# Kernel tuning notes

Measured on AMD Instinct MI355X. Metric: run time of the kernel, lower is better.

The kernel has to match this reference:

```python
import jax, jax.numpy as jnp
import numpy as np

EMBED_DIM = 1024
NUM_HEADS = 16
HEAD_DIM = EMBED_DIM // NUM_HEADS


def _rope_tables(seq_len, dim, dtype):
    # inv_freq over even indices of head_dim
    inv_freq = 1.0 / (10000.0 ** (jnp.arange(0, dim, 2, dtype=jnp.float32) / dim))
    t = jnp.arange(seq_len, dtype=jnp.float32)
    freqs = jnp.einsum('i,j->ij', t, inv_freq)            # [S, dim/2]
    emb = jnp.concatenate([freqs, freqs], axis=-1)        # [S, dim]
    return jnp.cos(emb).astype(dtype)[None], jnp.sin(emb).astype(dtype)[None]  # [1,S,dim]


def _rotate_half(x):
    x1, x2 = jnp.split(x, 2, axis=-1)
    return jnp.concatenate([-x2, x1], axis=-1)


def _apply_rope(x, cos, sin):
    return x * cos + _rotate_half(x) * sin


def setup_inputs() -> dict:
    key = jax.random.key(0)
    ks = jax.random.split(key, 9)
    S, B, E = 2048, 2, EMBED_DIM
    sc = 1.0 / np.sqrt(E)
    inp = {
        'query': jax.random.normal(ks[0], (S, B, E), jnp.float32),
        'Wq': jax.random.normal(ks[1], (E, E), jnp.float32) * sc,
        'bq': jnp.zeros((E,), jnp.float32),
        'Wk': jax.random.normal(ks[2], (E, E), jnp.float32) * sc,
        'bk': jnp.zeros((E,), jnp.float32),
        'Wv': jax.random.normal(ks[3], (E, E), jnp.float32) * sc,
        'bv': jnp.zeros((E,), jnp.float32),
        'Wo': jax.random.normal(ks[4], (E, E), jnp.float32) * sc,
        'bo': jnp.zeros((E,), jnp.float32),
    }
    return inp


def reference(query, Wq, bq, Wk, bk, Wv, bv, Wo, bo):
    tgt_len, bsz, E = query.shape
    H, hd = NUM_HEADS, HEAD_DIM
    scaling = hd ** (-0.5)

    # self-attention projections (torch Linear: x @ W.T + b)
    q = (query @ Wq.T + bq) * scaling
    k = query @ Wk.T + bk
    v = query @ Wv.T + bv

    # [S, B, E] -> [B*H, S, hd]
    def to_heads(x):
        return x.reshape(tgt_len, bsz * H, hd).transpose(1, 0, 2)

    q, k, v = to_heads(q), to_heads(k), to_heads(v)

    cos, sin = _rope_tables(tgt_len, hd, q.dtype)  # [1,S,hd]
    q = _apply_rope(q, cos, sin)
    k = _apply_rope(k, cos, sin)

    attn_weights = jnp.einsum('bqd,bkd->bqk', q, k)       # [B*H, S, S]
    attn_probs = jax.nn.softmax(attn_weights, axis=-1)
    attn = jnp.einsum('bqk,bkd->bqd', attn_probs, v)      # [B*H, S, hd]

    attn = attn.transpose(1, 0, 2).reshape(tgt_len, bsz, E)
    return attn @ Wo.T + bo
```

## Files before the change

### kernel.cpp

```cpp
#include <hip/hip_runtime.h>
#include <hip/hip_bf16.h>


typedef short shortx8 __attribute__((ext_vector_type(8)));
typedef float floatx4 __attribute__((ext_vector_type(4)));
typedef float floatx16 __attribute__((ext_vector_type(16)));

#define S_LEN 2048
#define BATCH 2
#define EMB 1024
#define NH 16
#define HD 64
#define BH 32
#define MROWS 4096
#define HEAD_STRIDE (S_LEN*HD)

#define QSCALE 0.1803368801111204f

#if __has_builtin(__builtin_amdgcn_exp2f)
#define EXP2(x) __builtin_amdgcn_exp2f(x)
#else
#define EXP2(x) exp2f(x)
#endif

__device__ __forceinline__ float b2f(unsigned short u) {
    union { unsigned int i; float f; } v; v.i = ((unsigned int)u) << 16; return v.f;
}
__device__ __forceinline__ unsigned short f2b(float f) {
    union { float f; unsigned int i; } v; v.f = f;
    unsigned int x = v.i;
    return (unsigned short)((x + 0x7fffu + ((x >> 16) & 1u)) >> 16);
}
__device__ __forceinline__ unsigned short f2b_fast(float f) {
    union { float f; unsigned int i; } v; v.f = f;
    return (unsigned short)((v.i + 0x8000u) >> 16);
}
__device__ __forceinline__ unsigned int fbits(float f) {
    union { float f; unsigned int i; } v; v.f = f; return v.i;
}
__device__ __forceinline__ unsigned int pack_bf16_2(float lo, float hi) {
    return __builtin_amdgcn_perm(fbits(hi) + 0x8000u, fbits(lo) + 0x8000u, 0x07060302u);
}
__device__ __forceinline__ shortx8 cvt8(const float* p) {
    floatx4 a = *(const floatx4*)p;
    floatx4 b = *(const floatx4*)(p + 4);
    shortx8 r;
    r[0] = (short)f2b(a[0]); r[1] = (short)f2b(a[1]);
    r[2] = (short)f2b(a[2]); r[3] = (short)f2b(a[3]);
    r[4] = (short)f2b(b[0]); r[5] = (short)f2b(b[1]);
    r[6] = (short)f2b(b[2]); r[7] = (short)f2b(b[3]);
    return r;
}
__device__ __forceinline__ shortx8 cvt8f(const float* p) {
    floatx4 a = *(const floatx4*)p;
    floatx4 b = *(const floatx4*)(p + 4);
    union { uint4 u; shortx8 s; } r;
    r.u.x = pack_bf16_2(a[0], a[1]);
    r.u.y = pack_bf16_2(a[2], a[3]);
    r.u.z = pack_bf16_2(b[0], b[1]);
    r.u.w = pack_bf16_2(b[2], b[3]);
    return r.s;
}
__device__ __forceinline__ void g2l16(const unsigned short* g, unsigned short* l) {
    __builtin_amdgcn_global_load_lds(
        (const __attribute__((address_space(1))) unsigned int*)(const void*)g,
        (__attribute__((address_space(3))) unsigned int*)(void*)l, 16, 0, 0);
}

__global__ __launch_bounds__(256) void prep(
    const float* __restrict__ X,
    const float* __restrict__ Wq, const float* __restrict__ Wk,
    const float* __restrict__ Wv,
    unsigned short* __restrict__ Xb, unsigned short* __restrict__ Wb,
    float* __restrict__ rtab)
{
    const int g = blockIdx.x * 256 + threadIdx.x;
    if (g < 65536) {
        const int s = g >> 5, j = g & 31;
        const float inv = expf(-(float)j * (9.210340371976184f / 32.0f));
        const float ang = (float)s * inv;
        rtab[s * 64 + j]      = cosf(ang);
        rtab[s * 64 + 32 + j] = sinf(ang);
    } else if (g < 458752) {
        const int h = g - 65536;
        const int seg = h >> 17;
        const int idx = (h & 131071) * 8;
        const float* W = (seg == 0) ? Wq : (seg == 1) ? Wk : Wv;
        *(shortx8*)&Wb[seg * 1048576 + idx] = cvt8(&W[idx]);
    } else {
        const int idx = (g - 458752) * 8;
        *(shortx8*)&Xb[idx] = cvt8(&X[idx]);
    }
}

__device__ __forceinline__ void qkv_epilogue(
    floatx4 (&acc)[4][4], int mat, int m0, int nn0, int wm, int wn,
    int qm, int quad, const float* bias, const float* rtab,
    unsigned short* dst)
{
    if (mat == 2) {
#pragma unroll
        for (int i = 0; i < 4; i++) {
#pragma unroll
            for (int j = 0; j < 4; j++) {
                const int colg = nn0 + wn + j * 16 + qm;
                const float bv_ = bias[colg];
                const int h = colg >> 6, d = colg & 63;
#pragma unroll
                for (int r = 0; r < 4; r++) {
                    const int rowg = m0 + wm + i * 16 + quad * 4 + r;
                    const int s = rowg >> 1, b = rowg & 1;
                    dst[((b * NH + h) * HD + d) * S_LEN + s] = f2b(acc[i][j][r] + bv_);
                }
            }
        }
    } else {
        const float scale = (mat == 0) ? QSCALE : 1.0f;
#pragma unroll
        for (int i = 0; i < 4; i++) {
#pragma unroll
            for (int jp = 0; jp < 2; jp++) {
                const int c1 = nn0 + wn + jp * 16 + qm;
                const float b1 = bias[c1], b2 = bias[c1 + 32];
                const int h = c1 >> 6;
                const int d1 = c1 & 63;
#pragma unroll
                for (int r = 0; r < 4; r++) {
                    const int rowg = m0 + wm + i * 16 + quad * 4 + r;
                    const int s = rowg >> 1, b = rowg & 1;
                    const float cs = rtab[s * 64 + d1];
                    const float sn = rtab[s * 64 + d1 + 32];
                    const float x1 = (acc[i][jp][r] + b1) * scale;
                    const float x2 = (acc[i][jp + 2][r] + b2) * scale;
                    unsigned short* base = &dst[((b * NH + h) * S_LEN + s) * HD];
                    base[d1]      = f2b(x1 * cs - x2 * sn);
                    base[d1 + 32] = f2b(x2 * cs + x1 * sn);
                }
            }
        }
    }
}

__global__ __launch_bounds__(256) void qkv_gemm_gl(
    const unsigned short* __restrict__ Xb,
    const unsigned short* __restrict__ Wb,
    const float* __restrict__ bq, const float* __restrict__ bk,
    const float* __restrict__ bv,
    const float* __restrict__ rtab,
    unsigned short* __restrict__ Qh, unsigned short* __restrict__ Kh,
    unsigned short* __restrict__ Vt)
{
    __shared__ unsigned short At[128 * 64];
    __shared__ unsigned short Bt[128 * 64];

    const int tid  = threadIdx.x;
    const int wave = tid >> 6, lane = tid & 63;
    const int wm = (wave >> 1) * 64, wn = (wave & 1) * 64;
    const int qm = lane & 15, quad = lane >> 4;

    const int m0  = blockIdx.x * 128;
    const int n0g = blockIdx.y * 128;
    const int mat = n0g >> 10;
    const int nn0 = n0g & 1023;

    const unsigned short* W = Wb + (size_t)mat * 1048576;
    const float* bias = (mat == 0) ? bq : (mat == 1) ? bk : bv;
    unsigned short* dst = (mat == 0) ? Qh : (mat == 1) ? Kh : Vt;

    floatx4 acc[4][4] = {};

    const int xs = qm & 7;

    for (int k0 = 0; k0 < EMB; k0 += 64) {
#pragma unroll
        for (int c = 0; c < 4; c++) {
            const int e   = (c * 256 + tid) * 8;
            const int row = e >> 6;
            const int gcol = (((e >> 3) & 7) ^ (row & 7)) * 8;
            g2l16(&Xb[(m0 + row) * EMB + k0 + gcol], &At[e]);
            g2l16(&W[(nn0 + row) * EMB + k0 + gcol], &Bt[e]);
        }
        __syncthreads();

#pragma unroll
        for (int kk = 0; kk < 2; kk++) {
            shortx8 a[4], b[4];
#pragma unroll
            for (int i = 0; i < 4; i++)
                a[i] = *(shortx8*)&At[(wm + i * 16 + qm) * 64 + (((kk * 4 + quad) ^ xs) * 8)];
#pragma unroll
            for (int j = 0; j < 4; j++)
                b[j] = *(shortx8*)&Bt[(wn + j * 16 + qm) * 64 + (((kk * 4 + quad) ^ xs) * 8)];
#pragma unroll
            for (int i = 0; i < 4; i++)
#pragma unroll
                for (int j = 0; j < 4; j++)
                    acc[i][j] = __builtin_amdgcn_mfma_f32_16x16x32_bf16(a[i], b[j], acc[i][j], 0, 0, 0);
        }
        __syncthreads();
    }

    qkv_epilogue(acc, mat, m0, nn0, wm, wn, qm, quad, bias, rtab, dst);
}

#define LDB 72

__global__ __launch_bounds__(256) void qkv_gemm_fb(
    const float* __restrict__ X,
    const unsigned short* __restrict__ Wb,
    const float* __restrict__ bq, const float* __restrict__ bk,
    const float* __restrict__ bv,
    const float* __restrict__ rtab,
    unsigned short* __restrict__ Qh, unsigned short* __restrict__ Kh,
    unsigned short* __restrict__ Vt)
{
    __shared__ unsigned short At[128 * LDB];
    __shared__ unsigned short Bt[128 * LDB];

    const int tid  = threadIdx.x;
    const int wave = tid >> 6, lane = tid & 63;
    const int wm = (wave >> 1) * 64, wn = (wave & 1) * 64;
    const int qm = lane & 15, quad = lane >> 4;

    const int m0  = blockIdx.x * 128;
    const int n0g = blockIdx.y * 128;
    const int mat = n0g >> 10;
    const int nn0 = n0g & 1023;

    const unsigned short* W = Wb + (size_t)mat * 1048576;
    const float* bias = (mat == 0) ? bq : (mat == 1) ? bk : bv;
    unsigned short* dst = (mat == 0) ? Qh : (mat == 1) ? Kh : Vt;

    const int r0 = tid >> 3;
    const int ko = (tid & 7) * 8;

    floatx4 acc[4][4] = {};

    for (int k0 = 0; k0 < EMB; k0 += 64) {
#pragma unroll
        for (int c = 0; c < 4; c++) {
            const int row = r0 + 32 * c;
            *(shortx8*)&At[row * LDB + ko] = cvt8(&X[(m0 + row) * EMB + k0 + ko]);
            *(shortx8*)&Bt[row * LDB + ko] = *(const shortx8*)&W[(nn0 + row) * EMB + k0 + ko];
        }
        __syncthreads();

#pragma unroll
        for (int kk = 0; kk < 2; kk++) {
            shortx8 a[4], b[4];
#pragma unroll
            for (int i = 0; i < 4; i++)
                a[i] = *(shortx8*)&At[(wm + i * 16 + qm) * LDB + kk * 32 + quad * 8];
#pragma unroll
            for (int j = 0; j < 4; j++)
                b[j] = *(shortx8*)&Bt[(wn + j * 16 + qm) * LDB + kk * 32 + quad * 8];
#pragma unroll
            for (int i = 0; i < 4; i++)
#pragma unroll
                for (int j = 0; j < 4; j++)
                    acc[i][j] = __builtin_amdgcn_mfma_f32_16x16x32_bf16(a[i], b[j], acc[i][j], 0, 0, 0);
        }
        __syncthreads();
    }

    qkv_epilogue(acc, mat, m0, nn0, wm, wn, qm, quad, bias, rtab, dst);
}

#define LDK 72
#define LDV 136
#define LDP 72

__global__ __launch_bounds__(512, 4) void attn_kernel(
    unsigned short* Qh,
    const unsigned short* __restrict__ Kh,
    const unsigned short* __restrict__ Vt)
{
    __shared__ unsigned short ldsK[128 * LDK];
    __shared__ unsigned short ldsVT[64 * LDV];
    __shared__ unsigned short ldsP[8 * 32 * LDP];

    const int tid  = threadIdx.x;
    const int wave = tid >> 6, lane = tid & 63;
    const int l32 = lane & 31, half = lane >> 5;
    const int qg = wave >> 1, ks = wave & 1;
    const int bh = blockIdx.y;
    const int qrow = blockIdx.x * 128 + qg * 32;

    unsigned short* Qp = Qh + bh * HEAD_STRIDE;
    const unsigned short* Kp = Kh + bh * HEAD_STRIDE;
    const unsigned short* Vp = Vt + bh * HEAD_STRIDE;

    shortx8 aq[4];
#pragma unroll
    for (int kk = 0; kk < 4; kk++)
        aq[kk] = *(const shortx8*)&Qp[(qrow + l32) * HD + kk * 16 + half * 8];

    floatx16 od0 = {}, od1 = {};
    float l_run = 0.0f;

    unsigned short* myP = &ldsP[wave * 32 * LDP];
    const int kb = ks * 64;

    const int kr = tid >> 3, ko = (tid & 7) * 8;
    const int vr = tid >> 4, vo = (tid & 15) * 8;

    for (int kt = 0; kt < S_LEN / 128; kt++) {
        const int kbase = kt * 128;
        *(shortx8*)&ldsK[kr * LDK + ko]        = *(const shortx8*)&Kp[(kbase + kr) * HD + ko];
        *(shortx8*)&ldsK[(kr + 64) * LDK + ko] = *(const shortx8*)&Kp[(kbase + kr + 64) * HD + ko];
        *(shortx8*)&ldsVT[vr * LDV + vo]        = *(const shortx8*)&Vp[vr * S_LEN + kbase + vo];
        *(shortx8*)&ldsVT[(vr + 32) * LDV + vo] = *(const shortx8*)&Vp[(vr + 32) * S_LEN + kbase + vo];
        __syncthreads();

#pragma unroll
        for (int sub = 0; sub < 2; sub++) {
            floatx16 sc = {};
#pragma unroll
            for (int kk = 0; kk < 4; kk++) {
                const shortx8 kf =
                    *(shortx8*)&ldsK[(kb + sub * 32 + l32) * LDK + kk * 16 + half * 8];
                sc = __builtin_amdgcn_mfma_f32_32x32x16_bf16(kf, aq[kk], sc, 0, 0, 0);
            }
#pragma unroll
            for (int c = 0; c < 4; c++) {
                const float p0 = EXP2(sc[4 * c + 0]);
                const float p1 = EXP2(sc[4 * c + 1]);
                const float p2 = EXP2(sc[4 * c + 2]);
                const float p3 = EXP2(sc[4 * c + 3]);
                l_run += (p0 + p1) + (p2 + p3);
                uint2 w;
                w.x = pack_bf16_2(p0, p1);
                w.y = pack_bf16_2(p2, p3);
                *(uint2*)&myP[l32 * LDP + sub * 32 + c * 8 + 4 * half] = w;
            }
        }

#pragma unroll
        for (int kc = 0; kc < 4; kc++) {
            const shortx8 ap = *(shortx8*)&myP[l32 * LDP + kc * 16 + half * 8];
            const shortx8 v0 = *(shortx8*)&ldsVT[l32 * LDV + kb + kc * 16 + half * 8];
            const shortx8 v1 = *(shortx8*)&ldsVT[(32 + l32) * LDV + kb + kc * 16 + half * 8];
            od0 = __builtin_amdgcn_mfma_f32_32x32x16_bf16(ap, v0, od0, 0, 0, 0);
            od1 = __builtin_amdgcn_mfma_f32_32x32x16_bf16(ap, v1, od1, 0, 0, 0);
        }
        __syncthreads();
    }

    l_run += __shfl_xor(l_run, 32, 64);

    float* ltab  = (float*)ldsVT + qg * 64 + ks * 32;
    float* odbuf = (float*)ldsP + qg * 2048;
    if (half == 0) ltab[l32] = l_run;
    if (ks == 1) {
#pragma unroll
        for (int g = 0; g < 16; g++) {
            const int row = (g & 3) + 8 * (g >> 2) + 4 * half;
            odbuf[row * 64 + l32]      = od0[g];
            odbuf[row * 64 + 32 + l32] = od1[g];
        }
    }
    __syncthreads();
    if (ks == 0) {
        const float* l0 = (float*)ldsVT + qg * 64;
        const float* l1 = l0 + 32;
#pragma unroll
        for (int g = 0; g < 16; g++) {
            const int row = (g & 3) + 8 * (g >> 2) + 4 * half;
            const float inv = 1.0f / (l0[row] + l1[row]);
            const float v0 = od0[g] + odbuf[row * 64 + l32];
            const float v1 = od1[g] + odbuf[row * 64 + 32 + l32];
            Qp[(qrow + row) * HD + l32]      = f2b(v0 * inv);
            Qp[(qrow + row) * HD + 32 + l32] = f2b(v1 * inv);
        }
    }
}

__global__ __launch_bounds__(256) void out_gemm(
    const unsigned short* __restrict__ O,
    const float* __restrict__ Wo, const float* __restrict__ bo,
    float* __restrict__ out)
{
    __shared__ unsigned short At[128 * LDB];
    __shared__ unsigned short Bt[64 * LDB];

    const int tid  = threadIdx.x;
    const int wave = tid >> 6, lane = tid & 63;
    const int wm = (wave >> 1) * 64, wn = (wave & 1) * 32;
    const int qm = lane & 15, quad = lane >> 4;
    const int m0 = blockIdx.x * 128;
    const int n0 = blockIdx.y * 64;

    const int r0 = tid >> 3;
    const int ko = (tid & 7) * 8;

    floatx4 acc[4][2] = {};

    for (int k0 = 0; k0 < EMB; k0 += 64) {
        const int k = k0 + ko;
#pragma unroll
        for (int c = 0; c < 4; c++) {
            const int row = r0 + 32 * c;
            const int m = m0 + row;
            *(shortx8*)&At[row * LDB + ko] =
                *(const shortx8*)&O[(((m & 1) * NH + (k >> 6)) * S_LEN + (m >> 1)) * HD + (k & 63)];
        }
#pragma unroll
        for (int c = 0; c < 2; c++) {
            const int row = r0 + 32 * c;
            *(shortx8*)&Bt[row * LDB + ko] = cvt8f(&Wo[(n0 + row) * EMB + k]);
        }
        __syncthreads();

#pragma unroll
        for (int kk = 0; kk < 2; kk++) {
            shortx8 a[4], b[2];
#pragma unroll
            for (int i = 0; i < 4; i++)
                a[i] = *(shortx8*)&At[(wm + i * 16 + qm) * LDB + kk * 32 + quad * 8];
#pragma unroll
            for (int j = 0; j < 2; j++)
                b[j] = *(shortx8*)&Bt[(wn + j * 16 + qm) * LDB + kk * 32 + quad * 8];
#pragma unroll
            for (int i = 0; i < 4; i++)
#pragma unroll
                for (int j = 0; j < 2; j++)
                    acc[i][j] = __builtin_amdgcn_mfma_f32_16x16x32_bf16(a[i], b[j], acc[i][j], 0, 0, 0);
        }
        __syncthreads();
    }

#pragma unroll
    for (int i = 0; i < 4; i++) {
#pragma unroll
        for (int j = 0; j < 2; j++) {
            const int colg = n0 + wn + j * 16 + qm;
            const float bv_ = bo[colg];
#pragma unroll
            for (int r = 0; r < 4; r++) {
                const int rowg = m0 + wm + i * 16 + quad * 4 + r;
                out[rowg * EMB + colg] = acc[i][j][r] + bv_;
            }
        }
    }
}

extern "C" void kernel_launch(void* const* d_in, const int* in_sizes, int n_in,
                              void* d_out, int out_size, void* d_ws, size_t ws_size,
                              hipStream_t stream) {
    const float* X  = (const float*)d_in[0];
    const float* Wq = (const float*)d_in[1];
    const float* bq = (const float*)d_in[2];
    const float* Wk = (const float*)d_in[3];
    const float* bk = (const float*)d_in[4];
    const float* Wv = (const float*)d_in[5];
    const float* bv = (const float*)d_in[6];
    const float* Wo = (const float*)d_in[7];
    const float* bo = (const float*)d_in[8];
    float* out = (float*)d_out;

    unsigned short* ws = (unsigned short*)d_ws;
    unsigned short* Vt  = ws;
    unsigned short* Qh  = ws + (size_t)BH * HEAD_STRIDE;
    unsigned short* Xb  = ws + (size_t)2 * BH * HEAD_STRIDE;
    unsigned short* Kh  = (unsigned short*)d_out;
    unsigned short* Wb  = (unsigned short*)d_out + 4194304;
    float*          Rt  = (float*)d_out + 3670016;

    const bool use_xb = ws_size >= (size_t)24 * 1024 * 1024;

    prep<<<dim3(use_xb ? 3840 : 1792), 256, 0, stream>>>(X, Wq, Wk, Wv, Xb, Wb, Rt);

    if (use_xb)
        qkv_gemm_gl<<<dim3(MROWS / 128, 3 * EMB / 128), 256, 0, stream>>>(
            Xb, Wb, bq, bk, bv, Rt, Qh, Kh, Vt);
    else
        qkv_gemm_fb<<<dim3(MROWS / 128, 3 * EMB / 128), 256, 0, stream>>>(
            X, Wb, bq, bk, bv, Rt, Qh, Kh, Vt);

    attn_kernel<<<dim3(S_LEN / 128, BH), 512, 0, stream>>>(Qh, Kh, Vt);
    out_gemm<<<dim3(MROWS / 128, EMB / 64), 256, 0, stream>>>(Qh, Wo, bo, out);
}
```

Before: 203.3 us.

## Keep softmax probabilities in registers via permlane swap and XOR-swizzle LDS tiles

Drops the per-wave LDS staging buffer for the probability matrix. The exp'd scores are now packed with v_cvt_pk_bf16_f32 and rearranged across half-waves with v_permlane32_swap, so they feed the PV MFMA directly from registers. K and V^T tiles move from padded row strides to an XOR-swizzled layout, which shrinks LDS usage while still avoiding bank conflicts. The epilogue buffers are remapped onto the single shared array, and correctness depends on the permlane fragment mapping matching the MFMA operand layout.

```diff
diff --git a/kernel.cpp b/kernel.cpp
--- a/kernel.cpp
+++ b/kernel.cpp
@@ -40,6 +40,21 @@
 }
 __device__ __forceinline__ unsigned int pack_bf16_2(float lo, float hi) {
     return __builtin_amdgcn_perm(fbits(hi) + 0x8000u, fbits(lo) + 0x8000u, 0x07060302u);
+}
+__device__ __forceinline__ unsigned int cvtpk_bf16(float lo, float hi) {
+    unsigned int r;
+    asm("v_cvt_pk_bf16_f32 %0, %1, %2" : "=v"(r) : "v"(lo), "v"(hi));
+    return r;
+}
+__device__ __forceinline__ void plswap(unsigned int &a, unsigned int &b) {
+#if __has_builtin(__builtin_amdgcn_permlane32_swap)
+    {
+        auto r = __builtin_amdgcn_permlane32_swap(a, b, false, false);
+        a = r[0]; b = r[1];
+    }
+#else
+    asm volatile("v_permlane32_swap_b32 %0, %1" : "+v"(a), "+v"(b));
+#endif
 }
 __device__ __forceinline__ shortx8 cvt8(const float* p) {
     floatx4 a = *(const floatx4*)p;
@@ -266,18 +281,16 @@
     qkv_epilogue(acc, mat, m0, nn0, wm, wn, qm, quad, bias, rtab, dst);
 }
 
-#define LDK 72
-#define LDV 136
-#define LDP 72
+#define SW8(c8, r) ((((c8) ^ ((r) & 7))) * 8)
 
 __global__ __launch_bounds__(512, 4) void attn_kernel(
     unsigned short* Qh,
     const unsigned short* __restrict__ Kh,
     const unsigned short* __restrict__ Vt)
 {
-    __shared__ unsigned short ldsK[128 * LDK];
-    __shared__ unsigned short ldsVT[64 * LDV];
-    __shared__ unsigned short ldsP[8 * 32 * LDP];
+    __shared__ __align__(16) unsigned short lds[8192 + 8192 + 512];
+    unsigned short* ldsK  = lds;
+    unsigned short* ldsVT = lds + 8192;
 
     const int tid  = threadIdx.x;
     const int wave = tid >> 6, lane = tid & 63;
@@ -298,18 +311,21 @@
     floatx16 od0 = {}, od1 = {};
     float l_run = 0.0f;
 
-    unsigned short* myP = &ldsP[wave * 32 * LDP];
     const int kb = ks * 64;
 
-    const int kr = tid >> 3, ko = (tid & 7) * 8;
-    const int vr = tid >> 4, vo = (tid & 15) * 8;
+    const int kr = tid >> 3, kc8 = tid & 7;
+    const int vr = tid >> 4, vc8 = tid & 15;
 
     for (int kt = 0; kt < S_LEN / 128; kt++) {
         const int kbase = kt * 128;
-        *(shortx8*)&ldsK[kr * LDK + ko]        = *(const shortx8*)&Kp[(kbase + kr) * HD + ko];
-        *(shortx8*)&ldsK[(kr + 64) * LDK + ko] = *(const shortx8*)&Kp[(kbase + kr + 64) * HD + ko];
-        *(shortx8*)&ldsVT[vr * LDV + vo]        = *(const shortx8*)&Vp[vr * S_LEN + kbase + vo];
-        *(shortx8*)&ldsVT[(vr + 32) * LDV + vo] = *(const shortx8*)&Vp[(vr + 32) * S_LEN + kbase + vo];
+        *(shortx8*)&ldsK[kr * 64 + SW8(kc8, kr)] =
+            *(const shortx8*)&Kp[(kbase + kr) * HD + kc8 * 8];
+        *(shortx8*)&ldsK[(kr + 64) * 64 + SW8(kc8, kr)] =
+            *(const shortx8*)&Kp[(kbase + kr + 64) * HD + kc8 * 8];
+        *(shortx8*)&ldsVT[vr * 128 + SW8(vc8, vr)] =
+            *(const shortx8*)&Vp[vr * S_LEN + kbase + vc8 * 8];
+        *(shortx8*)&ldsVT[(vr + 32) * 128 + SW8(vc8, vr)] =
+            *(const shortx8*)&Vp[(vr + 32) * S_LEN + kbase + vc8 * 8];
         __syncthreads();
 
 #pragma unroll
@@ -317,39 +333,42 @@
             floatx16 sc = {};
 #pragma unroll
             for (int kk = 0; kk < 4; kk++) {
-                const shortx8 kf =
-                    *(shortx8*)&ldsK[(kb + sub * 32 + l32) * LDK + kk * 16 + half * 8];
+                const shortx8 kf = *(shortx8*)&ldsK[
+                    (kb + sub * 32 + l32) * 64 + SW8(kk * 2 + half, l32)];
                 sc = __builtin_amdgcn_mfma_f32_32x32x16_bf16(kf, aq[kk], sc, 0, 0, 0);
             }
-#pragma unroll
-            for (int c = 0; c < 4; c++) {
-                const float p0 = EXP2(sc[4 * c + 0]);
-                const float p1 = EXP2(sc[4 * c + 1]);
-                const float p2 = EXP2(sc[4 * c + 2]);
-                const float p3 = EXP2(sc[4 * c + 3]);
-                l_run += (p0 + p1) + (p2 + p3);
-                uint2 w;
-                w.x = pack_bf16_2(p0, p1);
-                w.y = pack_bf16_2(p2, p3);
-                *(uint2*)&myP[l32 * LDP + sub * 32 + c * 8 + 4 * half] = w;
+            float p[16];
+#pragma unroll
+            for (int g = 0; g < 16; g++) p[g] = EXP2(sc[g]);
+#pragma unroll
+            for (int c = 0; c < 4; c++)
+                l_run += (p[4 * c] + p[4 * c + 1]) + (p[4 * c + 2] + p[4 * c + 3]);
+
+#pragma unroll
+            for (int f = 0; f < 2; f++) {
+                unsigned int d0 = cvtpk_bf16(p[8 * f + 0], p[8 * f + 1]);
+                unsigned int d2 = cvtpk_bf16(p[8 * f + 4], p[8 * f + 5]);
+                plswap(d0, d2);
+                unsigned int d1 = cvtpk_bf16(p[8 * f + 2], p[8 * f + 3]);
+                unsigned int d3 = cvtpk_bf16(p[8 * f + 6], p[8 * f + 7]);
+                plswap(d1, d3);
+                union { unsigned int u[4]; shortx8 s; } fr;
+                fr.u[0] = d0; fr.u[1] = d1; fr.u[2] = d2; fr.u[3] = d3;
+
+                const int c8 = (kb >> 3) + (sub * 2 + f) * 2 + half;
+                const shortx8 v0 = *(shortx8*)&ldsVT[l32 * 128 + SW8(c8, l32)];
+                const shortx8 v1 = *(shortx8*)&ldsVT[(32 + l32) * 128 + SW8(c8, l32)];
+                od0 = __builtin_amdgcn_mfma_f32_32x32x16_bf16(fr.s, v0, od0, 0, 0, 0);
+                od1 = __builtin_amdgcn_mfma_f32_32x32x16_bf16(fr.s, v1, od1, 0, 0, 0);
             }
         }
-
-#pragma unroll
-        for (int kc = 0; kc < 4; kc++) {
-            const shortx8 ap = *(shortx8*)&myP[l32 * LDP + kc * 16 + half * 8];
-            const shortx8 v0 = *(shortx8*)&ldsVT[l32 * LDV + kb + kc * 16 + half * 8];
-            const shortx8 v1 = *(shortx8*)&ldsVT[(32 + l32) * LDV + kb + kc * 16 + half * 8];
-            od0 = __builtin_amdgcn_mfma_f32_32x32x16_bf16(ap, v0, od0, 0, 0, 0);
-            od1 = __builtin_amdgcn_mfma_f32_32x32x16_bf16(ap, v1, od1, 0, 0, 0);
-        }
         __syncthreads();
     }
 
     l_run += __shfl_xor(l_run, 32, 64);
 
-    float* ltab  = (float*)ldsVT + qg * 64 + ks * 32;
-    float* odbuf = (float*)ldsP + qg * 2048;
+    float* ltab  = (float*)(lds + 16384) + qg * 64 + ks * 32;
+    float* odbuf = (float*)lds + qg * 2048;
     if (half == 0) ltab[l32] = l_run;
     if (ks == 1) {
 #pragma unroll
@@ -361,7 +380,7 @@
     }
     __syncthreads();
     if (ks == 0) {
-        const float* l0 = (float*)ldsVT + qg * 64;
+        const float* l0 = (float*)(lds + 16384) + qg * 64;
         const float* l1 = l0 + 32;
 #pragma unroll
         for (int g = 0; g < 16; g++) {
```

Result: no change. 200.9 us (-1.2%).
